# Kernel tuning notes

Measured on AMD Instinct MI355X. Metric: run time of the kernel, lower is better.

## Reference

```python
import jax, jax.numpy as jnp
import numpy as np
from jax import lax

WQ_MAX = 7.0    # int4 narrow symmetric range [-7, 7]
AQ_MAX = 15.0   # uint4 range [0, 15]
BN_EPS = 1e-5


def quant_weight(w):
    # per-output-channel symmetric int4 fake quant (OIHW, channel axis 0)
    s = jnp.max(jnp.abs(w), axis=(1, 2, 3), keepdims=True) / WQ_MAX
    s = jnp.maximum(s, 1e-8)
    return jnp.clip(jnp.round(w / s), -WQ_MAX, WQ_MAX) * s


def quant_relu(x, s):
    # ReLU fused with uint4 fake quant (clip at 0 subsumes ReLU)
    return jnp.clip(jnp.round(x / s), 0.0, AQ_MAX) * s


def conv2d(x, w, stride, pad, groups=1):
    return lax.conv_general_dilated(
        x, w, (stride, stride), [(pad, pad), (pad, pad)],
        feature_group_count=groups,
        dimension_numbers=('NCHW', 'OIHW', 'NCHW'))


def bn(x, g, b, m, v):
    inv = g / jnp.sqrt(v + BN_EPS)
    return x * inv[None, :, None, None] + (b - m * inv)[None, :, None, None]


def qconv_bn_qrelu(x, w, g, b, m, v, s, stride, pad, groups=1):
    x = conv2d(x, quant_weight(w), stride, pad, groups)
    return quant_relu(bn(x, g, b, m, v), s)


def setup_inputs() -> dict:
    key = jax.random.key(0)
    ks = jax.random.split(key, 8)
    d1, d2, oc = 32, 48, 64
    inp = {'x': jax.random.normal(ks[0], (8, 3, 512, 1024), dtype=jnp.float32)}

    def bn_params(c, tag):
        return {f'g{tag}': jnp.ones((c,), jnp.float32),
                f'b{tag}': jnp.zeros((c,), jnp.float32),
                f'm{tag}': jnp.zeros((c,), jnp.float32),
                f'v{tag}': jnp.ones((c,), jnp.float32)}

    inp['w1'] = 0.1 * jax.random.normal(ks[1], (d1, 3, 3, 3), jnp.float32)
    inp.update(bn_params(d1, 1)); inp['s1'] = jnp.float32(0.1)
    inp['wdw1'] = 0.1 * jax.random.normal(ks[2], (d1, 1, 3, 3), jnp.float32)
    inp.update(bn_params(d1, 2)); inp['s2'] = jnp.float32(0.1)
    inp['wpw1'] = 0.1 * jax.random.normal(ks[3], (d2, d1, 1, 1), jnp.float32)
    inp.update(bn_params(d2, 3)); inp['s3'] = jnp.float32(0.1)
    inp['wdw2'] = 0.1 * jax.random.normal(ks[4], (d2, 1, 3, 3), jnp.float32)
    inp.update(bn_params(d2, 4)); inp['s4'] = jnp.float32(0.1)
    inp['wpw2'] = 0.1 * jax.random.normal(ks[5], (oc, d2, 1, 1), jnp.float32)
    inp.update(bn_params(oc, 5)); inp['s5'] = jnp.float32(0.1)
    return inp


def reference(x, w1, g1, b1, m1, v1, s1,
              wdw1, g2, b2, m2, v2, s2,
              wpw1, g3, b3, m3, v3, s3,
              wdw2, g4, b4, m4, v4, s4,
              wpw2, g5, b5, m5, v5, s5):
    # _ConvBNReLU: 3x3 stride 2, padding 0
    x = qconv_bn_qrelu(x, w1, g1, b1, m1, v1, s1, stride=2, pad=0)
    # _DSConv 1: depthwise 3x3 s2 p1 (groups=32) + pointwise 1x1
    x = qconv_bn_qrelu(x, wdw1, g2, b2, m2, v2, s2, stride=2, pad=1, groups=32)
    x = qconv_bn_qrelu(x, wpw1, g3, b3, m3, v3, s3, stride=1, pad=0)
    # _DSConv 2: depthwise 3x3 s2 p1 (groups=48) + pointwise 1x1
    x = qconv_bn_qrelu(x, wdw2, g4, b4, m4, v4, s4, stride=2, pad=1, groups=48)
    x = qconv_bn_qrelu(x, wpw2, g5, b5, m5, v5, s5, stride=1, pad=0)
    return x  # [8, 64, 64, 128]
```

## Files before the change

### kernel.cpp

```cpp
#include <hip/hip_runtime.h>
#include <stdint.h>

#define AQ_MAX 15.0f
#define BN_EPS 1e-5f

__global__ __launch_bounds__(64) void prep_all(
    const float* __restrict__ wA, const float* __restrict__ gA,
    const float* __restrict__ bA, const float* __restrict__ mA,
    const float* __restrict__ vA,
    const float* __restrict__ wB, const float* __restrict__ gB,
    const float* __restrict__ bB, const float* __restrict__ mB,
    const float* __restrict__ vB,
    const float* __restrict__ wC, const float* __restrict__ gC,
    const float* __restrict__ bC, const float* __restrict__ mC,
    const float* __restrict__ vC,
    const float* __restrict__ wD, const float* __restrict__ gD,
    const float* __restrict__ bD, const float* __restrict__ mD,
    const float* __restrict__ vD,
    const float* __restrict__ wE, const float* __restrict__ gE,
    const float* __restrict__ bE, const float* __restrict__ mE,
    const float* __restrict__ vE,
    float* __restrict__ P) {
  int blk = blockIdx.x, t = threadIdx.x;
  const float *w, *g, *b, *m, *v;
  float *wq, *inv, *beta;
  int K, KP, c;
  if (blk < 32) {
    c = blk; w = wA; g = gA; b = bA; m = mA; v = vA; K = 27; KP = 28;
    wq = P + 0; inv = P + 6224; beta = P + 6256;
  } else if (blk < 64) {
    c = blk - 32; w = wB; g = gB; b = bB; m = mB; v = vB; K = 9; KP = 9;
    wq = P + 896; inv = P + 6288; beta = P + 6320;
  } else if (blk < 112) {
    c = blk - 64; w = wC; g = gC; b = bC; m = mC; v = vC; K = 32; KP = 32;
    wq = P + 1184; inv = P + 6352; beta = P + 6400;
  } else if (blk < 160) {
    c = blk - 112; w = wD; g = gD; b = bD; m = mD; v = vD; K = 9; KP = 9;
    wq = P + 2720; inv = P + 6448; beta = P + 6496;
  } else {
    c = blk - 160; w = wE; g = gE; b = bE; m = mE; v = vE; K = 48; KP = 48;
    wq = P + 3152; inv = P + 6544; beta = P + 6608;
  }
  const float* wc = w + (size_t)c * K;
  float a = (t < K) ? fabsf(wc[t]) : 0.0f;
#pragma unroll
  for (int off = 32; off >= 1; off >>= 1) a = fmaxf(a, __shfl_xor(a, off));
  float s = fmaxf(a / 7.0f, 1e-8f);
  if (t < K) {
    float q = rintf(wc[t] / s);
    q = fminf(7.0f, fmaxf(-7.0f, q));
    wq[(size_t)c * KP + t] = q * s;
  } else if (t < KP) {
    wq[(size_t)c * KP + t] = 0.0f;
  }
  if (t == 0) {
    float iv = g[c] / sqrtf(v[c] + BN_EPS);
    inv[c] = iv;
    beta[c] = b[c] - m[c] * iv;
  }
}

__global__ __launch_bounds__(256) void stage1_kernel(
    const float* __restrict__ x, const float* __restrict__ P,
    const float* __restrict__ s1p, uint8_t* __restrict__ out) {
  int tid = blockIdx.x * 256 + threadIdx.x;
  int gx = tid & 255;
  int t2 = tid >> 8;
  int oy = t2 % 255;
  int n = t2 / 255;
  float s1 = *s1p;
  int ix0 = gx * 4, iy = 2 * oy;
  bool tailok = (ix0 + 4) < 1024;
  float r[9][5];
#pragma unroll
  for (int ic = 0; ic < 3; ic++)
#pragma unroll
    for (int kh = 0; kh < 3; kh++) {
      const float* bp = x + (((size_t)(n * 3 + ic)) * 512 + (iy + kh)) * 1024 + ix0;
      float4 f = *(const float4*)bp;
      int s = ic * 3 + kh;
      r[s][0] = f.x; r[s][1] = f.y; r[s][2] = f.z; r[s][3] = f.w;
      r[s][4] = tailok ? bp[4] : 0.0f;
    }
  size_t obase = (((size_t)n * 32) * 255 + oy) * 512 + gx * 2;
#pragma unroll 2
  for (int oc = 0; oc < 32; oc++) {
    const float* wp = P + oc * 28;
    float w[27];
#pragma unroll
    for (int j = 0; j < 27; j++) w[j] = wp[j];
    float a0 = 0.0f, a1 = 0.0f;
#pragma unroll
    for (int s = 0; s < 9; s++) {
#pragma unroll
      for (int kw = 0; kw < 3; kw++) {
        float wv = w[s * 3 + kw];
        a0 = fmaf(r[s][0 + kw], wv, a0);
        a1 = fmaf(r[s][2 + kw], wv, a1);
      }
    }
    float iv = P[6224 + oc], bt = P[6256 + oc];
    float y0 = fmaf(a0, iv, bt), y1 = fmaf(a1, iv, bt);
    uint32_t q0 = (uint32_t)fminf(AQ_MAX, fmaxf(0.0f, rintf(y0 / s1)));
    uint32_t q1 = (uint32_t)fminf(AQ_MAX, fmaxf(0.0f, rintf(y1 / s1)));
    uint16_t pk = (uint16_t)(q0 | (q1 << 8));
    *(uint16_t*)(out + obase + (size_t)oc * (255 * 512)) = pk;
  }
}

template <int C, int IH, int IWL, int IWP, int OH, int OW>
__global__ __launch_bounds__(256) void dw_kernel(
    const uint8_t* __restrict__ in, const float* __restrict__ wq,
    const float* __restrict__ inv, const float* __restrict__ beta,
    const float* __restrict__ sin_p, const float* __restrict__ sout_p,
    uint8_t* __restrict__ out) {
  constexpr int GX = OW / 4;
  int tid = blockIdx.x * 256 + threadIdx.x;
  int oxg = tid % GX;
  int t2 = tid / GX;
  int oy = t2 % OH;
  int t3 = t2 / OH;
  int c = __builtin_amdgcn_readfirstlane(t3 % C);
  int n = __builtin_amdgcn_readfirstlane(t3 / C);
  float s_in = *sin_p, s_out = *sout_p;
  const float* wc = wq + c * 9;
  float w[9];
#pragma unroll
  for (int j = 0; j < 9; j++) w[j] = wc[j];
  float iv = inv[c], bt = beta[c];
  int c0 = oxg * 8;
  const uint8_t* chan = in + ((size_t)(n * C + c)) * IH * IWP;
  float xr[3][9];
#pragma unroll
  for (int kh = 0; kh < 3; kh++) {
    int iy = 2 * oy + kh - 1;
    if (iy >= 0 && iy < IH) {
      const uint8_t* rp = chan + (size_t)iy * IWP;
      uint2 u = *(const uint2*)(rp + c0);
      xr[kh][0] = (oxg > 0) ? (float)rp[c0 - 1] : 0.0f;
#pragma unroll
      for (int j = 0; j < 4; j++) xr[kh][1 + j] = (float)((u.x >> (8 * j)) & 255u);
#pragma unroll
      for (int j = 0; j < 4; j++) xr[kh][5 + j] = (float)((u.y >> (8 * j)) & 255u);
      if (IWL < IWP && oxg == GX - 1) xr[kh][8] = 0.0f;
    } else {
#pragma unroll
      for (int j = 0; j < 9; j++) xr[kh][j] = 0.0f;
    }
  }
#pragma unroll
  for (int kh = 0; kh < 3; kh++)
#pragma unroll
    for (int j = 0; j < 9; j++) xr[kh][j] *= s_in;
  float acc[4] = {0, 0, 0, 0};
#pragma unroll
  for (int kh = 0; kh < 3; kh++)
#pragma unroll
    for (int kw = 0; kw < 3; kw++) {
      float wv = w[kh * 3 + kw];
#pragma unroll
      for (int p = 0; p < 4; p++) acc[p] = fmaf(xr[kh][2 * p + kw], wv, acc[p]);
    }
  uint32_t pack = 0;
#pragma unroll
  for (int p = 0; p < 4; p++) {
    float y = fmaf(acc[p], iv, bt);
    float q = fminf(AQ_MAX, fmaxf(0.0f, rintf(y / s_out)));
    pack |= ((uint32_t)q) << (8 * p);
  }
  *(uint32_t*)(out + ((size_t)(n * C + c) * OH + oy) * OW + c0 / 2) = pack;
}

template <int IC, int OC, int CHUNK, int HW, bool FINAL>
__global__ __launch_bounds__(256) void pw_kernel(
    const uint8_t* __restrict__ in, const float* __restrict__ Pw,
    const float* __restrict__ Pinv, const float* __restrict__ Pbeta,
    const float* __restrict__ sin_p, const float* __restrict__ sout_p,
    void* __restrict__ outv) {
  constexpr int NCH = OC / CHUNK;
  constexpr int PG = HW / 2;
  int bid = blockIdx.x;
  int chunk = bid % NCH;
  int pb = bid / NCH;
  int tpx = pb * 256 + threadIdx.x;
  int px0 = (tpx % PG) * 2;
  int n = __builtin_amdgcn_readfirstlane(tpx / PG);
  float s_in = *sin_p, s_out = *sout_p;
  const uint8_t* ib = in + (size_t)n * IC * HW + px0;
  float xa[IC], xb[IC];
#pragma unroll
  for (int ic = 0; ic < IC; ic++) {
    uint16_t u = *(const uint16_t*)(ib + (size_t)ic * HW);
    xa[ic] = (float)(u & 255u) * s_in;
    xb[ic] = (float)(u >> 8) * s_in;
  }
  int oc0 = chunk * CHUNK;
#pragma unroll 2
  for (int oc = oc0; oc < oc0 + CHUNK; oc++) {
    const float* wp = Pw + oc * IC;
    float w[IC];
#pragma unroll
    for (int ic = 0; ic < IC; ic++) w[ic] = wp[ic];
    float a0 = 0, a1 = 0;
#pragma unroll
    for (int ic = 0; ic < IC; ic++) {
      a0 = fmaf(xa[ic], w[ic], a0);
      a1 = fmaf(xb[ic], w[ic], a1);
    }
    float iv = Pinv[oc], bt = Pbeta[oc];
    float y0 = fmaf(a0, iv, bt), y1 = fmaf(a1, iv, bt);
    float q0 = fminf(AQ_MAX, fmaxf(0.0f, rintf(y0 / s_out)));
    float q1 = fminf(AQ_MAX, fmaxf(0.0f, rintf(y1 / s_out)));
    if (FINAL) {
      float2 o;
      o.x = q0 * s_out; o.y = q1 * s_out;
      *(float2*)((float*)outv + (size_t)(n * OC + oc) * HW + px0) = o;
    } else {
      uint16_t pk = (uint16_t)((uint32_t)q0 | ((uint32_t)q1 << 8));
      *(uint16_t*)((uint8_t*)outv + (size_t)(n * OC + oc) * HW + px0) = pk;
    }
  }
}

extern "C" void kernel_launch(void* const* d_in, const int* in_sizes, int n_in,
                              void* d_out, int out_size, void* d_ws, size_t ws_size,
                              hipStream_t stream) {
  const float* x    = (const float*)d_in[0];
  const float* w1   = (const float*)d_in[1];
  const float* g1   = (const float*)d_in[2];
  const float* b1   = (const float*)d_in[3];
  const float* m1   = (const float*)d_in[4];
  const float* v1   = (const float*)d_in[5];
  const float* s1   = (const float*)d_in[6];
  const float* wdw1 = (const float*)d_in[7];
  const float* g2   = (const float*)d_in[8];
  const float* b2   = (const float*)d_in[9];
  const float* m2   = (const float*)d_in[10];
  const float* v2   = (const float*)d_in[11];
  const float* s2   = (const float*)d_in[12];
  const float* wpw1 = (const float*)d_in[13];
  const float* g3   = (const float*)d_in[14];
  const float* b3   = (const float*)d_in[15];
  const float* m3   = (const float*)d_in[16];
  const float* v3   = (const float*)d_in[17];
  const float* s3   = (const float*)d_in[18];
  const float* wdw2 = (const float*)d_in[19];
  const float* g4   = (const float*)d_in[20];
  const float* b4   = (const float*)d_in[21];
  const float* m4   = (const float*)d_in[22];
  const float* v4   = (const float*)d_in[23];
  const float* s4   = (const float*)d_in[24];
  const float* wpw2 = (const float*)d_in[25];
  const float* g5   = (const float*)d_in[26];
  const float* b5   = (const float*)d_in[27];
  const float* m5   = (const float*)d_in[28];
  const float* v5   = (const float*)d_in[29];
  const float* s5   = (const float*)d_in[30];

  float* P = (float*)d_ws;
  float* wq2  = P + 896;
  float* wq3  = P + 1184;
  float* wq4  = P + 2720;
  float* wq5  = P + 3152;
  float* inv2 = P + 6288, *beta2 = P + 6320;
  float* inv3 = P + 6352, *beta3 = P + 6400;
  float* inv4 = P + 6448, *beta4 = P + 6496;
  float* inv5 = P + 6544, *beta5 = P + 6608;

  uint8_t* ws8 = (uint8_t*)d_ws;
  uint8_t* x1 = ws8 + 32768;
  uint8_t* x2 = x1 + 33423360;
  uint8_t* x3 = x2 + 8388608;
  uint8_t* x4 = ws8 + 32768;

  prep_all<<<224, 64, 0, stream>>>(w1, g1, b1, m1, v1,
                                   wdw1, g2, b2, m2, v2,
                                   wpw1, g3, b3, m3, v3,
                                   wdw2, g4, b4, m4, v4,
                                   wpw2, g5, b5, m5, v5, P);

  stage1_kernel<<<2040, 256, 0, stream>>>(x, P, s1, x1);
  dw_kernel<32, 255, 511, 512, 128, 256>
      <<<8192, 256, 0, stream>>>(x1, wq2, inv2, beta2, s1, s2, x2);
  pw_kernel<32, 48, 24, 32768, false>
      <<<1024, 256, 0, stream>>>(x2, wq3, inv3, beta3, s2, s3, x3);
  dw_kernel<48, 128, 256, 256, 64, 128>
      <<<3072, 256, 0, stream>>>(x3, wq4, inv4, beta4, s3, s4, x4);
  pw_kernel<48, 64, 8, 8192, true>
      <<<1024, 256, 0, stream>>>(x4, wq5, inv5, beta5, s4, s5, (float*)d_out);
}
```

Before: 118.9 us.

## Double-buffer weight loads and widen stage1 to four outputs per thread

Stage1 now computes four output columns per thread instead of two, reading 8+1 input floats per row and halving the grid. Both stage1 and the first pointwise kernel prefetch the next output channel's weights into a second register buffer, issued between sched_barriers in the middle of the current channel's FMAs so load latency overlaps compute. This costs more registers per thread and fewer waves in the stage1 launch.

```diff
diff --git a/kernel.cpp b/kernel.cpp
--- a/kernel.cpp
+++ b/kernel.cpp
@@ -60,51 +60,80 @@
   }
 }
 
+#define S1_ROW(W, S)                                              \
+  {                                                               \
+    float wv0 = W[(S)*3], wv1 = W[(S)*3 + 1], wv2 = W[(S)*3 + 2]; \
+    a0 = fmaf(r[S][0], wv0, a0); a1 = fmaf(r[S][2], wv0, a1);     \
+    a2 = fmaf(r[S][4], wv0, a2); a3 = fmaf(r[S][6], wv0, a3);     \
+    a0 = fmaf(r[S][1], wv1, a0); a1 = fmaf(r[S][3], wv1, a1);     \
+    a2 = fmaf(r[S][5], wv1, a2); a3 = fmaf(r[S][7], wv1, a3);     \
+    a0 = fmaf(r[S][2], wv2, a0); a1 = fmaf(r[S][4], wv2, a1);     \
+    a2 = fmaf(r[S][6], wv2, a2); a3 = fmaf(r[S][8], wv2, a3);     \
+  }
+
+#define S1_LOADW(W, IV, BT, OCIDX)                              \
+  {                                                             \
+    _Pragma("unroll") for (int tq = 0; tq < 7; tq++) {          \
+      float4 f = *(const float4*)(P + (OCIDX)*28 + 4 * tq);     \
+      W[4*tq] = f.x; W[4*tq+1] = f.y;                           \
+      W[4*tq+2] = f.z; W[4*tq+3] = f.w;                         \
+    }                                                           \
+    IV = P[6224 + (OCIDX)];                                     \
+    BT = P[6256 + (OCIDX)];                                     \
+  }
+
+#define S1_BODY(W, IV, BT, OCIDX, ...)                                     \
+  {                                                                        \
+    float a0 = 0, a1 = 0, a2 = 0, a3 = 0;                                  \
+    S1_ROW(W, 0);                                                          \
+    __builtin_amdgcn_sched_barrier(0);                                     \
+    __VA_ARGS__                                                            \
+    __builtin_amdgcn_sched_barrier(0);                                     \
+    S1_ROW(W, 1); S1_ROW(W, 2); S1_ROW(W, 3); S1_ROW(W, 4);                \
+    S1_ROW(W, 5); S1_ROW(W, 6); S1_ROW(W, 7); S1_ROW(W, 8);                \
+    float y0 = fmaf(a0, IV, BT), y1 = fmaf(a1, IV, BT);                    \
+    float y2 = fmaf(a2, IV, BT), y3 = fmaf(a3, IV, BT);                    \
+    uint32_t q0 = (uint32_t)fminf(AQ_MAX, fmaxf(0.0f, rintf(y0 / s1)));    \
+    uint32_t q1 = (uint32_t)fminf(AQ_MAX, fmaxf(0.0f, rintf(y1 / s1)));    \
+    uint32_t q2 = (uint32_t)fminf(AQ_MAX, fmaxf(0.0f, rintf(y2 / s1)));    \
+    uint32_t q3 = (uint32_t)fminf(AQ_MAX, fmaxf(0.0f, rintf(y3 / s1)));    \
+    *(uint32_t*)(out + obase + (size_t)(OCIDX) * (255 * 512)) =            \
+        q0 | (q1 << 8) | (q2 << 16) | (q3 << 24);                          \
+  }
+
 __global__ __launch_bounds__(256) void stage1_kernel(
     const float* __restrict__ x, const float* __restrict__ P,
     const float* __restrict__ s1p, uint8_t* __restrict__ out) {
   int tid = blockIdx.x * 256 + threadIdx.x;
-  int gx = tid & 255;
-  int t2 = tid >> 8;
+  int gx = tid & 127;
+  int t2 = tid >> 7;
   int oy = t2 % 255;
   int n = t2 / 255;
   float s1 = *s1p;
-  int ix0 = gx * 4, iy = 2 * oy;
-  bool tailok = (ix0 + 4) < 1024;
-  float r[9][5];
+  int ix0 = gx * 8, iy = 2 * oy;
+  bool tailok = (ix0 + 8) < 1024;
+  float r[9][9];
 #pragma unroll
   for (int ic = 0; ic < 3; ic++)
 #pragma unroll
     for (int kh = 0; kh < 3; kh++) {
       const float* bp = x + (((size_t)(n * 3 + ic)) * 512 + (iy + kh)) * 1024 + ix0;
-      float4 f = *(const float4*)bp;
+      float4 f0 = *(const float4*)bp;
+      float4 f1 = *(const float4*)(bp + 4);
       int s = ic * 3 + kh;
-      r[s][0] = f.x; r[s][1] = f.y; r[s][2] = f.z; r[s][3] = f.w;
-      r[s][4] = tailok ? bp[4] : 0.0f;
-    }
-  size_t obase = (((size_t)n * 32) * 255 + oy) * 512 + gx * 2;
-#pragma unroll 2
-  for (int oc = 0; oc < 32; oc++) {
-    const float* wp = P + oc * 28;
-    float w[27];
-#pragma unroll
-    for (int j = 0; j < 27; j++) w[j] = wp[j];
-    float a0 = 0.0f, a1 = 0.0f;
-#pragma unroll
-    for (int s = 0; s < 9; s++) {
-#pragma unroll
-      for (int kw = 0; kw < 3; kw++) {
-        float wv = w[s * 3 + kw];
-        a0 = fmaf(r[s][0 + kw], wv, a0);
-        a1 = fmaf(r[s][2 + kw], wv, a1);
-      }
-    }
-    float iv = P[6224 + oc], bt = P[6256 + oc];
-    float y0 = fmaf(a0, iv, bt), y1 = fmaf(a1, iv, bt);
-    uint32_t q0 = (uint32_t)fminf(AQ_MAX, fmaxf(0.0f, rintf(y0 / s1)));
-    uint32_t q1 = (uint32_t)fminf(AQ_MAX, fmaxf(0.0f, rintf(y1 / s1)));
-    uint16_t pk = (uint16_t)(q0 | (q1 << 8));
-    *(uint16_t*)(out + obase + (size_t)oc * (255 * 512)) = pk;
+      r[s][0] = f0.x; r[s][1] = f0.y; r[s][2] = f0.z; r[s][3] = f0.w;
+      r[s][4] = f1.x; r[s][5] = f1.y; r[s][6] = f1.z; r[s][7] = f1.w;
+      r[s][8] = tailok ? bp[8] : 0.0f;
+    }
+  size_t obase = (((size_t)n * 32) * 255 + oy) * 512 + gx * 4;
+  float wA[28], wB[28], ivA, btA, ivB, btB;
+  S1_LOADW(wA, ivA, btA, 0);
+#pragma unroll
+  for (int i = 0; i < 32; i += 2) {
+    S1_BODY(wA, ivA, btA, i, { S1_LOADW(wB, ivB, btB, i + 1); });
+    S1_BODY(wB, ivB, btB, i + 1, {
+      if (i + 2 < 32) S1_LOADW(wA, ivA, btA, i + 2);
+    });
   }
 }
 
@@ -171,7 +200,45 @@
   *(uint32_t*)(out + ((size_t)(n * C + c) * OH + oy) * OW + c0 / 2) = pack;
 }
 
-template <int IC, int OC, int CHUNK, int HW, bool FINAL>
+#define PW_LOADW(W, IV, BT, OCIDX)                                   \
+  {                                                                  \
+    _Pragma("unroll") for (int tq = 0; tq < IC / 4; tq++) {          \
+      float4 f = *(const float4*)(Pw + (size_t)(OCIDX)*IC + 4 * tq); \
+      W[4*tq] = f.x; W[4*tq+1] = f.y;                                \
+      W[4*tq+2] = f.z; W[4*tq+3] = f.w;                              \
+    }                                                                \
+    IV = Pinv[(OCIDX)];                                              \
+    BT = Pbeta[(OCIDX)];                                             \
+  }
+
+#define PW_BODY(W, IV, BT, OCIDX, ...)                                       \
+  {                                                                          \
+    float a0 = 0, a1 = 0;                                                    \
+    _Pragma("unroll") for (int ic = 0; ic < 8; ic++) {                       \
+      a0 = fmaf(xa[ic], W[ic], a0);                                          \
+      a1 = fmaf(xb[ic], W[ic], a1);                                          \
+    }                                                                        \
+    __builtin_amdgcn_sched_barrier(0);                                       \
+    __VA_ARGS__                                                              \
+    __builtin_amdgcn_sched_barrier(0);                                       \
+    _Pragma("unroll") for (int ic = 8; ic < IC; ic++) {                      \
+      a0 = fmaf(xa[ic], W[ic], a0);                                          \
+      a1 = fmaf(xb[ic], W[ic], a1);                                          \
+    }                                                                        \
+    float y0 = fmaf(a0, IV, BT), y1 = fmaf(a1, IV, BT);                      \
+    float q0 = fminf(AQ_MAX, fmaxf(0.0f, rintf(y0 / s_out)));                \
+    float q1 = fminf(AQ_MAX, fmaxf(0.0f, rintf(y1 / s_out)));                \
+    if (FINAL) {                                                             \
+      float2 o;                                                              \
+      o.x = q0 * s_out; o.y = q1 * s_out;                                    \
+      *(float2*)((float*)outv + ((size_t)n * OC + (OCIDX)) * HW + px0) = o;  \
+    } else {                                                                 \
+      uint16_t pk = (uint16_t)((uint32_t)q0 | ((uint32_t)q1 << 8));          \
+      *(uint16_t*)((uint8_t*)outv + ((size_t)n * OC + (OCIDX)) * HW + px0) = pk; \
+    }                                                                        \
+  }
+
+template <int IC, int OC, int CHUNK, int HW, bool FINAL, bool DB>
 __global__ __launch_bounds__(256) void pw_kernel(
     const uint8_t* __restrict__ in, const float* __restrict__ Pw,
     const float* __restrict__ Pinv, const float* __restrict__ Pbeta,
@@ -195,29 +262,41 @@
     xb[ic] = (float)(u >> 8) * s_in;
   }
   int oc0 = chunk * CHUNK;
+  if (DB) {
+    float wA[IC], wB[IC], ivA, btA, ivB, btB;
+    PW_LOADW(wA, ivA, btA, oc0);
+#pragma unroll
+    for (int i = 0; i < CHUNK; i += 2) {
+      PW_BODY(wA, ivA, btA, oc0 + i, { PW_LOADW(wB, ivB, btB, oc0 + i + 1); });
+      PW_BODY(wB, ivB, btB, oc0 + i + 1, {
+        if (i + 2 < CHUNK) PW_LOADW(wA, ivA, btA, oc0 + i + 2);
+      });
+    }
+  } else {
 #pragma unroll 2
-  for (int oc = oc0; oc < oc0 + CHUNK; oc++) {
-    const float* wp = Pw + oc * IC;
-    float w[IC];
-#pragma unroll
-    for (int ic = 0; ic < IC; ic++) w[ic] = wp[ic];
-    float a0 = 0, a1 = 0;
-#pragma unroll
-    for (int ic = 0; ic < IC; ic++) {
-      a0 = fmaf(xa[ic], w[ic], a0);
-      a1 = fmaf(xb[ic], w[ic], a1);
-    }
-    float iv = Pinv[oc], bt = Pbeta[oc];
-    float y0 = fmaf(a0, iv, bt), y1 = fmaf(a1, iv, bt);
-    float q0 = fminf(AQ_MAX, fmaxf(0.0f, rintf(y0 / s_out)));
-    float q1 = fminf(AQ_MAX, fmaxf(0.0f, rintf(y1 / s_out)));
-    if (FINAL) {
-      float2 o;
-      o.x = q0 * s_out; o.y = q1 * s_out;
-      *(float2*)((float*)outv + (size_t)(n * OC + oc) * HW + px0) = o;
-    } else {
-      uint16_t pk = (uint16_t)((uint32_t)q0 | ((uint32_t)q1 << 8));
-      *(uint16_t*)((uint8_t*)outv + (size_t)(n * OC + oc) * HW + px0) = pk;
+    for (int oc = oc0; oc < oc0 + CHUNK; oc++) {
+      const float* wp = Pw + (size_t)oc * IC;
+      float w[IC];
+#pragma unroll
+      for (int ic = 0; ic < IC; ic++) w[ic] = wp[ic];
+      float a0 = 0, a1 = 0;
+#pragma unroll
+      for (int ic = 0; ic < IC; ic++) {
+        a0 = fmaf(xa[ic], w[ic], a0);
+        a1 = fmaf(xb[ic], w[ic], a1);
+      }
+      float iv = Pinv[oc], bt = Pbeta[oc];
+      float y0 = fmaf(a0, iv, bt), y1 = fmaf(a1, iv, bt);
+      float q0 = fminf(AQ_MAX, fmaxf(0.0f, rintf(y0 / s_out)));
+      float q1 = fminf(AQ_MAX, fmaxf(0.0f, rintf(y1 / s_out)));
+      if (FINAL) {
+        float2 o;
+        o.x = q0 * s_out; o.y = q1 * s_out;
+        *(float2*)((float*)outv + ((size_t)n * OC + oc) * HW + px0) = o;
+      } else {
+        uint16_t pk = (uint16_t)((uint32_t)q0 | ((uint32_t)q1 << 8));
+        *(uint16_t*)((uint8_t*)outv + ((size_t)n * OC + oc) * HW + px0) = pk;
+      }
     }
   }
 }
@@ -279,13 +358,13 @@
                                    wdw2, g4, b4, m4, v4,
                                    wpw2, g5, b5, m5, v5, P);
 
-  stage1_kernel<<<2040, 256, 0, stream>>>(x, P, s1, x1);
+  stage1_kernel<<<1020, 256, 0, stream>>>(x, P, s1, x1);
   dw_kernel<32, 255, 511, 512, 128, 256>
       <<<8192, 256, 0, stream>>>(x1, wq2, inv2, beta2, s1, s2, x2);
-  pw_kernel<32, 48, 24, 32768, false>
+  pw_kernel<32, 48, 24, 32768, false, true>
       <<<1024, 256, 0, stream>>>(x2, wq3, inv3, beta3, s2, s3, x3);
   dw_kernel<48, 128, 256, 256, 64, 128>
       <<<3072, 256, 0, stream>>>(x3, wq4, inv4, beta4, s3, s4, x4);
-  pw_kernel<48, 64, 8, 8192, true>
+  pw_kernel<48, 64, 8, 8192, true, false>
       <<<1024, 256, 0, stream>>>(x4, wq5, inv5, beta5, s4, s5, (float*)d_out);
 }
```

After: 119.2 us. Within noise of the previous version (+0.2%).

## Fuse depthwise and pointwise stages through shared-memory tiles

Applied to the files above, without the earlier changes.

Merges each depthwise 3x3 conv with the following pointwise 1x1 conv into one kernel. The depthwise output for a spatial tile across all channels is kept in LDS and consumed directly by the pointwise stage. This removes the intermediate global writes and reads and two kernel launches. In exchange the grids get much smaller (512 and 256 blocks), each thread now loops over all output channels, and there is an extra block-wide barrier, so occupancy and parallelism drop.

```diff
diff --git a/kernel.cpp b/kernel.cpp
--- a/kernel.cpp
+++ b/kernel.cpp
@@ -108,116 +108,135 @@
   }
 }
 
-template <int C, int IH, int IWL, int IWP, int OH, int OW>
-__global__ __launch_bounds__(256) void dw_kernel(
-    const uint8_t* __restrict__ in, const float* __restrict__ wq,
-    const float* __restrict__ inv, const float* __restrict__ beta,
-    const float* __restrict__ sin_p, const float* __restrict__ sout_p,
-    uint8_t* __restrict__ out) {
-  constexpr int GX = OW / 4;
-  int tid = blockIdx.x * 256 + threadIdx.x;
-  int oxg = tid % GX;
-  int t2 = tid / GX;
-  int oy = t2 % OH;
-  int t3 = t2 / OH;
-  int c = __builtin_amdgcn_readfirstlane(t3 % C);
-  int n = __builtin_amdgcn_readfirstlane(t3 / C);
-  float s_in = *sin_p, s_out = *sout_p;
-  const float* wc = wq + c * 9;
-  float w[9];
-#pragma unroll
-  for (int j = 0; j < 9; j++) w[j] = wc[j];
-  float iv = inv[c], bt = beta[c];
-  int c0 = oxg * 8;
-  const uint8_t* chan = in + ((size_t)(n * C + c)) * IH * IWP;
-  float xr[3][9];
-#pragma unroll
-  for (int kh = 0; kh < 3; kh++) {
-    int iy = 2 * oy + kh - 1;
-    if (iy >= 0 && iy < IH) {
-      const uint8_t* rp = chan + (size_t)iy * IWP;
-      uint2 u = *(const uint2*)(rp + c0);
-      xr[kh][0] = (oxg > 0) ? (float)rp[c0 - 1] : 0.0f;
-#pragma unroll
-      for (int j = 0; j < 4; j++) xr[kh][1 + j] = (float)((u.x >> (8 * j)) & 255u);
-#pragma unroll
-      for (int j = 0; j < 4; j++) xr[kh][5 + j] = (float)((u.y >> (8 * j)) & 255u);
-      if (IWL < IWP && oxg == GX - 1) xr[kh][8] = 0.0f;
-    } else {
-#pragma unroll
-      for (int j = 0; j < 9; j++) xr[kh][j] = 0.0f;
-    }
-  }
-#pragma unroll
-  for (int kh = 0; kh < 3; kh++)
-#pragma unroll
-    for (int j = 0; j < 9; j++) xr[kh][j] *= s_in;
-  float acc[4] = {0, 0, 0, 0};
-#pragma unroll
-  for (int kh = 0; kh < 3; kh++)
-#pragma unroll
-    for (int kw = 0; kw < 3; kw++) {
-      float wv = w[kh * 3 + kw];
-#pragma unroll
-      for (int p = 0; p < 4; p++) acc[p] = fmaf(xr[kh][2 * p + kw], wv, acc[p]);
-    }
-  uint32_t pack = 0;
-#pragma unroll
-  for (int p = 0; p < 4; p++) {
-    float y = fmaf(acc[p], iv, bt);
-    float q = fminf(AQ_MAX, fmaxf(0.0f, rintf(y / s_out)));
-    pack |= ((uint32_t)q) << (8 * p);
-  }
-  *(uint32_t*)(out + ((size_t)(n * C + c) * OH + oy) * OW + c0 / 2) = pack;
-}
-
-template <int IC, int OC, int CHUNK, int HW, bool FINAL>
-__global__ __launch_bounds__(256) void pw_kernel(
-    const uint8_t* __restrict__ in, const float* __restrict__ Pw,
-    const float* __restrict__ Pinv, const float* __restrict__ Pbeta,
-    const float* __restrict__ sin_p, const float* __restrict__ sout_p,
-    void* __restrict__ outv) {
-  constexpr int NCH = OC / CHUNK;
-  constexpr int PG = HW / 2;
+template <int C, int OC, int IH, int IWL, int IWP, int OH, int OW,
+          int TH, int TW, bool FINAL>
+__global__ __launch_bounds__(256) void dwpw_kernel(
+    const uint8_t* __restrict__ in,
+    const float* __restrict__ Wdw, const float* __restrict__ Idw,
+    const float* __restrict__ Bdw,
+    const float* __restrict__ Wpw, const float* __restrict__ Ipw,
+    const float* __restrict__ Bpw,
+    const float* __restrict__ sin_p, const float* __restrict__ smid_p,
+    const float* __restrict__ sout_p, void* __restrict__ outv) {
+  constexpr int TS = TW + 4;
+  __shared__ uint8_t mid[C * TH * TS];
+  constexpr int TILES_X = OW / TW, TILES_Y = OH / TH;
   int bid = blockIdx.x;
-  int chunk = bid % NCH;
-  int pb = bid / NCH;
-  int tpx = pb * 256 + threadIdx.x;
-  int px0 = (tpx % PG) * 2;
-  int n = __builtin_amdgcn_readfirstlane(tpx / PG);
-  float s_in = *sin_p, s_out = *sout_p;
-  const uint8_t* ib = in + (size_t)n * IC * HW + px0;
-  float xa[IC], xb[IC];
-#pragma unroll
-  for (int ic = 0; ic < IC; ic++) {
-    uint16_t u = *(const uint16_t*)(ib + (size_t)ic * HW);
-    xa[ic] = (float)(u & 255u) * s_in;
-    xb[ic] = (float)(u >> 8) * s_in;
-  }
-  int oc0 = chunk * CHUNK;
+  int tx = bid % TILES_X;
+  int t2b = bid / TILES_X;
+  int ty = t2b % TILES_Y;
+  int n = t2b / TILES_Y;
+  int X0 = tx * TW, Y0 = ty * TH;
+  float s_in = *sin_p, s_mid = *smid_p, s_out = *sout_p;
+
+  constexpr int QPC = TH * (TW / 4);
+  constexpr int NITER = (C * QPC) / 256;
+  for (int k = 0; k < NITER; k++) {
+    int t = threadIdx.x + k * 256;
+    int ch = __builtin_amdgcn_readfirstlane(t / QPC);
+    int r = t % QPC;
+    int py = r / (TW / 4);
+    int qx = r % (TW / 4);
+    int oy = Y0 + py;
+    int ox0 = X0 + qx * 4;
+    int c0 = 2 * ox0;
+    const float* wc = Wdw + ch * 9;
+    float w[9];
+#pragma unroll
+    for (int j = 0; j < 9; j++) w[j] = wc[j];
+    float iv = Idw[ch], bt = Bdw[ch];
+    const uint8_t* chan = in + ((size_t)(n * C + ch)) * IH * IWP;
+    float xr[3][9];
+#pragma unroll
+    for (int kh = 0; kh < 3; kh++) {
+      int iy = 2 * oy + kh - 1;
+      if (iy >= 0 && iy < IH) {
+        const uint8_t* rp = chan + (size_t)iy * IWP;
+        uint2 u = *(const uint2*)(rp + c0);
+        xr[kh][0] = (ox0 > 0) ? (float)rp[c0 - 1] : 0.0f;
+#pragma unroll
+        for (int j = 0; j < 4; j++) xr[kh][1 + j] = (float)((u.x >> (8 * j)) & 255u);
+#pragma unroll
+        for (int j = 0; j < 4; j++) xr[kh][5 + j] = (float)((u.y >> (8 * j)) & 255u);
+        if (c0 + 8 > IWL) xr[kh][8] = 0.0f;
+      } else {
+#pragma unroll
+        for (int j = 0; j < 9; j++) xr[kh][j] = 0.0f;
+      }
+    }
+#pragma unroll
+    for (int kh = 0; kh < 3; kh++)
+#pragma unroll
+      for (int j = 0; j < 9; j++) xr[kh][j] *= s_in;
+    float acc[4] = {0, 0, 0, 0};
+#pragma unroll
+    for (int kh = 0; kh < 3; kh++)
+#pragma unroll
+      for (int kw = 0; kw < 3; kw++) {
+        float wv = w[kh * 3 + kw];
+#pragma unroll
+        for (int p = 0; p < 4; p++) acc[p] = fmaf(xr[kh][2 * p + kw], wv, acc[p]);
+      }
+    uint32_t pack = 0;
+#pragma unroll
+    for (int p = 0; p < 4; p++) {
+      float y = fmaf(acc[p], iv, bt);
+      float q = fminf(AQ_MAX, fmaxf(0.0f, rintf(y / s_mid)));
+      pack |= ((uint32_t)q) << (8 * p);
+    }
+    *(uint32_t*)&mid[ch * (TH * TS) + py * TS + qx * 4] = pack;
+  }
+  __syncthreads();
+
+  if (FINAL) {
+    int py = threadIdx.x / TW, px = threadIdx.x % TW;
+    float xa[C];
+#pragma unroll
+    for (int ic = 0; ic < C; ic++)
+      xa[ic] = (float)mid[ic * (TH * TS) + py * TS + px] * s_mid;
+    size_t ob = ((size_t)n * OC) * (OH * OW) + (size_t)(Y0 + py) * OW + X0 + px;
 #pragma unroll 2
-  for (int oc = oc0; oc < oc0 + CHUNK; oc++) {
-    const float* wp = Pw + oc * IC;
-    float w[IC];
-#pragma unroll
-    for (int ic = 0; ic < IC; ic++) w[ic] = wp[ic];
-    float a0 = 0, a1 = 0;
-#pragma unroll
-    for (int ic = 0; ic < IC; ic++) {
-      a0 = fmaf(xa[ic], w[ic], a0);
-      a1 = fmaf(xb[ic], w[ic], a1);
-    }
-    float iv = Pinv[oc], bt = Pbeta[oc];
-    float y0 = fmaf(a0, iv, bt), y1 = fmaf(a1, iv, bt);
-    float q0 = fminf(AQ_MAX, fmaxf(0.0f, rintf(y0 / s_out)));
-    float q1 = fminf(AQ_MAX, fmaxf(0.0f, rintf(y1 / s_out)));
-    if (FINAL) {
-      float2 o;
-      o.x = q0 * s_out; o.y = q1 * s_out;
-      *(float2*)((float*)outv + (size_t)(n * OC + oc) * HW + px0) = o;
-    } else {
+    for (int oc = 0; oc < OC; oc++) {
+      const float* wp = Wpw + (size_t)oc * C;
+      float w[C];
+#pragma unroll
+      for (int ic = 0; ic < C; ic++) w[ic] = wp[ic];
+      float a0 = 0;
+#pragma unroll
+      for (int ic = 0; ic < C; ic++) a0 = fmaf(xa[ic], w[ic], a0);
+      float y0 = fmaf(a0, Ipw[oc], Bpw[oc]);
+      float q0 = fminf(AQ_MAX, fmaxf(0.0f, rintf(y0 / s_out)));
+      ((float*)outv)[ob + (size_t)oc * (OH * OW)] = q0 * s_out;
+    }
+  } else {
+    int pxi = threadIdx.x * 2;
+    int py = pxi / TW, px = pxi % TW;
+    float xa[C], xb[C];
+#pragma unroll
+    for (int ic = 0; ic < C; ic++) {
+      uint16_t u = *(const uint16_t*)&mid[ic * (TH * TS) + py * TS + px];
+      xa[ic] = (float)(u & 255u) * s_mid;
+      xb[ic] = (float)(u >> 8) * s_mid;
+    }
+    size_t ob = ((size_t)n * OC) * (OH * OW) + (size_t)(Y0 + py) * OW + X0 + px;
+#pragma unroll 2
+    for (int oc = 0; oc < OC; oc++) {
+      const float* wp = Wpw + (size_t)oc * C;
+      float w[C];
+#pragma unroll
+      for (int ic = 0; ic < C; ic++) w[ic] = wp[ic];
+      float a0 = 0, a1 = 0;
+#pragma unroll
+      for (int ic = 0; ic < C; ic++) {
+        a0 = fmaf(xa[ic], w[ic], a0);
+        a1 = fmaf(xb[ic], w[ic], a1);
+      }
+      float y0 = fmaf(a0, Ipw[oc], Bpw[oc]);
+      float y1 = fmaf(a1, Ipw[oc], Bpw[oc]);
+      float q0 = fminf(AQ_MAX, fmaxf(0.0f, rintf(y0 / s_out)));
+      float q1 = fminf(AQ_MAX, fmaxf(0.0f, rintf(y1 / s_out)));
       uint16_t pk = (uint16_t)((uint32_t)q0 | ((uint32_t)q1 << 8));
-      *(uint16_t*)((uint8_t*)outv + (size_t)(n * OC + oc) * HW + px0) = pk;
+      *(uint16_t*)((uint8_t*)outv + ob + (size_t)oc * (OH * OW)) = pk;
     }
   }
 }
@@ -269,9 +288,7 @@
 
   uint8_t* ws8 = (uint8_t*)d_ws;
   uint8_t* x1 = ws8 + 32768;
-  uint8_t* x2 = x1 + 33423360;
-  uint8_t* x3 = x2 + 8388608;
-  uint8_t* x4 = ws8 + 32768;
+  uint8_t* x3 = x1 + 33423360;
 
   prep_all<<<224, 64, 0, stream>>>(w1, g1, b1, m1, v1,
                                    wdw1, g2, b2, m2, v2,
@@ -280,12 +297,10 @@
                                    wpw2, g5, b5, m5, v5, P);
 
   stage1_kernel<<<2040, 256, 0, stream>>>(x, P, s1, x1);
-  dw_kernel<32, 255, 511, 512, 128, 256>
-      <<<8192, 256, 0, stream>>>(x1, wq2, inv2, beta2, s1, s2, x2);
-  pw_kernel<32, 48, 24, 32768, false>
-      <<<1024, 256, 0, stream>>>(x2, wq3, inv3, beta3, s2, s3, x3);
-  dw_kernel<48, 128, 256, 256, 64, 128>
-      <<<3072, 256, 0, stream>>>(x3, wq4, inv4, beta4, s3, s4, x4);
-  pw_kernel<48, 64, 8, 8192, true>
-      <<<1024, 256, 0, stream>>>(x4, wq5, inv5, beta5, s4, s5, (float*)d_out);
+  dwpw_kernel<32, 48, 255, 511, 512, 128, 256, 16, 32, false>
+      <<<512, 256, 0, stream>>>(x1, wq2, inv2, beta2, wq3, inv3, beta3,
+                                s1, s2, s3, x3);
+  dwpw_kernel<48, 64, 128, 256, 256, 64, 128, 8, 32, true>
+      <<<256, 256, 0, stream>>>(x3, wq4, inv4, beta4, wq5, inv5, beta5,
+                                s3, s4, s5, (float*)d_out);
 }
```

Result: slower. 161.0 us (+35.4%).
